# Optimization experiments

Measured on AMD Instinct MI355X. Metric: run time of the kernel, lower is better.

## Reference

```python
import jax, jax.numpy as jnp
import numpy as np

N = 50000      # nodes
E = 800000     # edges
D = 128        # input_dim = nb_hidden = emb_dim
A = 4          # nb_edge_types (edge attr dim)
H = 2          # heads (MyGATConv default)
G = 128        # number of graphs (g.batch)
NEG = 0.2      # leaky_relu negative slope
L = 3          # nb_layers


def _glorot(key, shape):
    lim = np.sqrt(6.0 / (shape[-2] + shape[-1]))
    return jax.random.uniform(key, shape, minval=-lim, maxval=lim, dtype=jnp.float32)


def setup_inputs():
    key = jax.random.key(0)
    ks = jax.random.split(key, 20)
    inp = {
        "x": jax.random.normal(ks[0], (N, D), jnp.float32),
        "edge_index": jax.random.randint(ks[1], (2, E), 0, N, dtype=jnp.int32),
        "edge_attr": jax.random.normal(ks[2], (E, A), jnp.float32),
        "batch": jnp.sort(jax.random.randint(ks[3], (N,), 0, G, dtype=jnp.int32)),
    }
    for l in range(L):
        inp[f"linN{l}"] = _glorot(ks[4 + 4 * l], (D, H * D))
        inp[f"linE{l}"] = _glorot(ks[5 + 4 * l], (A, H * A))
        inp[f"att{l}"] = _glorot(ks[6 + 4 * l], (1, H, 2 * D + A))
        inp[f"bias{l}"] = jnp.zeros((H * D,), jnp.float32)
    inp["fw"] = _glorot(ks[16], (D, 1))
    inp["fb"] = jnp.zeros((1,), jnp.float32)
    return inp


def _gat_layer(x_in, e_in, src, dst, linN, linE, att, bias):
    n = x_in.shape[0]
    x = (x_in @ linN + bias).reshape(n, H, D)              # [N,H,D]
    e = (e_in @ linE).reshape(-1, H, A)                    # [E,H,A]
    # alpha = (cat([x_i, x_j, e], -1) * att).sum(-1); x_i = x[src], x_j = x[dst]
    ai = jnp.einsum('nhc,hc->nh', x, att[0, :, :D])        # per-node, gathered at src
    aj = jnp.einsum('nhc,hc->nh', x, att[0, :, D:2 * D])   # per-node, gathered at dst
    ae = jnp.einsum('ehc,hc->eh', e, att[0, :, 2 * D:])
    alpha = jax.nn.leaky_relu(ai[src] + aj[dst] + ae, NEG)  # [E,H]
    # segment softmax over targets (edge_index[1])
    amax = jax.ops.segment_max(alpha, dst, num_segments=n)
    ex = jnp.exp(alpha - amax[dst])
    denom = jax.ops.segment_sum(ex, dst, num_segments=n)
    alpha = ex / denom[dst]
    # PyG propagate: message = alpha * x[src], scatter-add at dst
    msg = alpha[:, :, None] * x[src]                       # [E,H,D]
    out = jax.ops.segment_sum(msg, dst, num_segments=n) + x
    # concat=False -> mean over heads, then ReLU
    return jax.nn.relu(out.mean(axis=1)), jax.nn.relu(e.mean(axis=1))


def reference(x, edge_index, edge_attr, batch,
              linN0, linE0, att0, bias0,
              linN1, linE1, att1, bias1,
              linN2, linE2, att2, bias2,
              fw, fb):
    src, dst = edge_index[0], edge_index[1]
    params = [(linN0, linE0, att0, bias0),
              (linN1, linE1, att1, bias1),
              (linN2, linE2, att2, bias2)]
    h, e = x, edge_attr
    for (lN, lE, at, b) in params:
        h, e = _gat_layer(h, e, src, dst, lN, lE, at, b)
    pooled = jax.ops.segment_sum(h, batch, num_segments=G)  # global_add_pool -> [G,D]
    y = (pooled @ fw + fb).squeeze(-1)                      # [G]
    return y
```

## Files before the change

### kernel.cpp

```cpp
#include <hip/hip_runtime.h>
#include <hip/hip_bf16.h>

#define DD 128
#define AA 4
#define HH 2

typedef short short8 __attribute__((ext_vector_type(8)));
typedef float f32x4 __attribute__((ext_vector_type(4)));

__device__ inline unsigned short f2bf(float f) {
    unsigned u = __float_as_uint(f);
    unsigned r = (u + 0x7fffu + ((u >> 16) & 1u)) >> 16;
    return (unsigned short)r;
}
__device__ inline float4 unpack_bf16x4(uint2 v) {
    float4 r;
    r.x = __uint_as_float(v.x << 16);
    r.y = __uint_as_float(v.x & 0xffff0000u);
    r.z = __uint_as_float(v.y << 16);
    r.w = __uint_as_float(v.y & 0xffff0000u);
    return r;
}
__device__ inline uint2 pack_bf16x4(float a, float b, float c, float d) {
    uint2 p;
    p.x = (unsigned)f2bf(a) | ((unsigned)f2bf(b) << 16);
    p.y = (unsigned)f2bf(c) | ((unsigned)f2bf(d) << 16);
    return p;
}


__global__ void rank_kernel(const int* __restrict__ dst, int* __restrict__ cnt,
                            int* __restrict__ rank, int E) {
    int e = blockIdx.x * blockDim.x + threadIdx.x;
    if (e < E) rank[e] = atomicAdd(&cnt[dst[e]], 1);
}

__global__ __launch_bounds__(256) void scan1(const int* __restrict__ cnt,
                                             int* __restrict__ bsum, int N,
                                             float* __restrict__ y,
                                             const float* __restrict__ fb) {
    __shared__ int wsh[4];
    int b = blockIdx.x, t = threadIdx.x;
    int lane = t & 63, w = t >> 6;
    if (b == 0 && t < 128) y[t] = fb[0];
    int base = b * 1024;
    int v = 0;
    #pragma unroll
    for (int i = 0; i < 4; ++i) {
        int idx = base + i * 256 + t;
        v += (idx < N) ? cnt[idx] : 0;
    }
    #pragma unroll
    for (int o = 32; o; o >>= 1) v += __shfl_xor(v, o);
    if (lane == 0) wsh[w] = v;
    __syncthreads();
    if (t == 0) bsum[b] = wsh[0] + wsh[1] + wsh[2] + wsh[3];
}

__global__ __launch_bounds__(256) void scan3(const int* __restrict__ cnt,
                                             const int* __restrict__ bsum,
                                             int* __restrict__ row_off,
                                             int N, int NB, int E) {
    __shared__ int wtot[4];
    __shared__ int carry;
    int b = blockIdx.x, t = threadIdx.x;
    int lane = t & 63, w = t >> 6;
    if (w == 0) {
        int v = (lane < NB) ? bsum[lane] : 0;
        int x = v;
        #pragma unroll
        for (int o = 1; o < 64; o <<= 1) {
            int u = __shfl_up(x, o);
            if (lane >= o) x += u;
        }
        int base = (b == 0) ? 0 : __shfl(x, b - 1);
        if (lane == 0) carry = base;
    }
    if (b == 0 && t == 0) row_off[N] = E;
    __syncthreads();
    int base = b * 1024;
    #pragma unroll
    for (int it = 0; it < 4; ++it) {
        int idx = base + it * 256 + t;
        int v = (idx < N) ? cnt[idx] : 0;
        int x = v;
        #pragma unroll
        for (int o = 1; o < 64; o <<= 1) {
            int u = __shfl_up(x, o);
            if (lane >= o) x += u;
        }
        if (lane == 63) wtot[w] = x;
        __syncthreads();
        int woff = 0;
        for (int i = 0; i < w; ++i) woff += wtot[i];
        int c = carry;
        __syncthreads();
        if (t == 255) carry = c + woff + x;
        int ex = c + woff + x - v;
        if (idx < N) row_off[idx] = ex;
        __syncthreads();
    }
}

__global__ void perm_kernel(const int* __restrict__ src, const int* __restrict__ dst,
                            const int* __restrict__ rank,
                            const int* __restrict__ row_off,
                            int2* __restrict__ perm2, int E) {
    int e = blockIdx.x * blockDim.x + threadIdx.x;
    if (e >= E) return;
    int2 v; v.x = e; v.y = src[e];
    perm2[row_off[dst[e]] + rank[e]] = v;
}


__device__ inline void edge_stage(const float4& ev, const float* __restrict__ linE,
                                  const float* __restrict__ att, float2& ae, float4& enext) {
    float eh[8];
    #pragma unroll
    for (int c = 0; c < 8; ++c)
        eh[c] = ev.x * linE[c] + ev.y * linE[8 + c] + ev.z * linE[16 + c] + ev.w * linE[24 + c];
    float a0 = 0.f, a1 = 0.f;
    #pragma unroll
    for (int a = 0; a < 4; ++a) {
        a0 += eh[a]     * att[2 * DD + a];
        a1 += eh[4 + a] * att[(2 * DD + AA) + 2 * DD + a];
    }
    ae.x = a0; ae.y = a1;
    enext.x = fmaxf(0.5f * (eh[0] + eh[4]), 0.f);
    enext.y = fmaxf(0.5f * (eh[1] + eh[5]), 0.f);
    enext.z = fmaxf(0.5f * (eh[2] + eh[6]), 0.f);
    enext.w = fmaxf(0.5f * (eh[3] + eh[7]), 0.f);
}

__global__ __launch_bounds__(256) void prep_fused(
        const float* __restrict__ ein, const int2* __restrict__ perm2,
        const float* __restrict__ linE0, const float* __restrict__ att0,
        const float* __restrict__ linE1, const float* __restrict__ att1,
        const float* __restrict__ linE2, const float* __restrict__ att2,
        float2* __restrict__ ae0, float2* __restrict__ ae1, float2* __restrict__ ae2,
        int E, int ebE,
        const float* __restrict__ X, uint2* __restrict__ As, int N, int ebA,
        const float* __restrict__ W0, const float* __restrict__ W1,
        const float* __restrict__ W2, unsigned short* __restrict__ Bs) {
    int b = blockIdx.x;
    if (b < ebE) {
        int p = b * 256 + threadIdx.x;
        if (p >= E) return;
        int e = perm2[p].x;
        float4 ev = ((const float4*)ein)[e];
        float2 ae; float4 en;
        edge_stage(ev, linE0, att0, ae, en); ae0[p] = ae;
        edge_stage(en, linE1, att1, ae, ev); ae1[p] = ae;
        edge_stage(ev, linE2, att2, ae, en); ae2[p] = ae;
    } else if (b < ebE + ebA) {
        int t = (b - ebE) * 256 + threadIdx.x;
        if (t >= N * 32) return;
        int r = t >> 5, kq4 = t & 31;
        float4 v = ((const float4*)X)[t];
        int g = r >> 4, m = r & 15;
        int ks = kq4 >> 3, q = (kq4 >> 1) & 3;
        int cell = ((g * 4 + ks) * 4 + q) * 16 + m;
        As[cell * 2 + (kq4 & 1)] = pack_bf16x4(v.x, v.y, v.z, v.w);
    } else {
        int t = (b - ebE - ebA) * 256 + threadIdx.x;
        if (t >= 3 * 128 * 64) return;
        int l = t / (128 * 64);
        int r = t - l * (128 * 64);
        const float* W = (l == 0) ? W0 : (l == 1) ? W1 : W2;
        unsigned short* B = Bs + (size_t)l * 128 * 256;
        int k = r >> 6, c4g = r & 63;
        float4 v = ((const float4*)W)[r];
        int ct = c4g >> 2, n0 = (c4g & 3) * 4;
        int ks = k >> 5, q = (k >> 3) & 3, j = k & 7;
        int cellbase = ((ct * 4 + ks) * 4 + q) * 16 + n0;
        B[(cellbase + 0) * 8 + j] = f2bf(v.x);
        B[(cellbase + 1) * 8 + j] = f2bf(v.y);
        B[(cellbase + 2) * 8 + j] = f2bf(v.z);
        B[(cellbase + 3) * 8 + j] = f2bf(v.w);
    }
}


__global__ __launch_bounds__(256) void gemm_mfma(const short8* __restrict__ As,
                                                 const short8* __restrict__ Bs,
                                                 const float* __restrict__ bias,
                                                 const float* __restrict__ att,
                                                 uint2* __restrict__ xhb,
                                                 float* __restrict__ aiaj, int Ngroups) {
    __shared__ __align__(16) unsigned short sh[4][16 * 132];
    int w = threadIdx.x >> 6;
    int flat = blockIdx.x * 4 + w;
    int wid = flat >> 1, half = flat & 1;
    int lane = threadIdx.x & 63;
    if (wid >= Ngroups) return;
    int q = lane >> 4, m = lane & 15;

    const short8* Ag = As + (size_t)wid * 256;
    f32x4 acc[8];
    #pragma unroll
    for (int c8 = 0; c8 < 8; ++c8) acc[c8] = (f32x4){0.f, 0.f, 0.f, 0.f};

    #pragma unroll
    for (int ks = 0; ks < 4; ++ks) {
        short8 a = Ag[ks * 64 + lane];
        #pragma unroll
        for (int c8 = 0; c8 < 8; ++c8) {
            short8 b = Bs[(half * 8 + c8) * 256 + ks * 64 + lane];
            acc[c8] = __builtin_amdgcn_mfma_f32_16x16x32_bf16(a, b, acc[c8], 0, 0, 0);
        }
    }

    const float* atth = att + half * (2 * DD + AA);
    float ai[4] = {}, aj[4] = {};
    #pragma unroll
    for (int c8 = 0; c8 < 8; ++c8) {
        int col = c8 * 16 + m;
        float aS = atth[col];
        float aD = atth[DD + col];
        float bv = bias[(half * 8 + c8) * 16 + m];
        #pragma unroll
        for (int reg = 0; reg < 4; ++reg) {
            float val = acc[c8][reg] + bv;
            sh[w][(q * 4 + reg) * 132 + col] = f2bf(val);
            ai[reg] += val * aS;
            aj[reg] += val * aD;
        }
    }
    #pragma unroll
    for (int o = 1; o < 16; o <<= 1) {
        #pragma unroll
        for (int reg = 0; reg < 4; ++reg) {
            ai[reg] += __shfl_xor(ai[reg], o);
            aj[reg] += __shfl_xor(aj[reg], o);
        }
    }
    if (m == 0) {
        #pragma unroll
        for (int reg = 0; reg < 4; ++reg) {
            int row = wid * 16 + q * 4 + reg;
            aiaj[row * 4 + half] = ai[reg];
            aiaj[row * 4 + 2 + half] = aj[reg];
        }
    }
    #pragma unroll
    for (int r2 = 0; r2 < 8; ++r2) {
        int row = r2 * 2 + (lane >> 5);
        uint2 v = *(const uint2*)&sh[w][row * 132 + (lane & 31) * 4];
        xhb[(size_t)(wid * 16 + row) * 64 + half * 32 + (lane & 31)] = v;
    }
}


__global__ __launch_bounds__(256) void aggregate(const uint2* __restrict__ xhb,
                                                 const float* __restrict__ aiaj,
                                                 const float2* __restrict__ ae,
                                                 const int* __restrict__ row_off,
                                                 const int2* __restrict__ perm2,
                                                 uint2* __restrict__ hshuf,
                                                 const float* __restrict__ fw,
                                                 float* __restrict__ pdots, int N) {
    int w = threadIdx.x >> 6;
    int d = blockIdx.x * 4 + w;
    int lane = threadIdx.x & 63;
    if (d >= N) return;
    int s0 = row_off[d], s1 = row_off[d + 1];
    int deg = s1 - s0;
    const float2* aiaj2 = (const float2*)aiaj;
    float2 ajv = aiaj2[d * 2 + 1];
    float4 xd = unpack_bf16x4(xhb[(size_t)d * 64 + lane]);

    __shared__ float lex[4][64][2];
    __shared__ int lsrc[4][64];
    float4 acc = {0.f, 0.f, 0.f, 0.f};
    float den0 = 0.f, den1 = 0.f;
    int head = lane >> 5;

    for (int c = 0; c < deg; c += 64) {
        int n = min(64, deg - c);
        if (lane < n) {
            int p = s0 + c + lane;
            int s = perm2[p].y;
            float2 aiv = aiaj2[s * 2];
            float2 aev = ae[p];
            float a0 = aiv.x + ajv.x + aev.x; a0 = a0 > 0.f ? a0 : 0.2f * a0;
            float a1 = aiv.y + ajv.y + aev.y; a1 = a1 > 0.f ? a1 : 0.2f * a1;
            float e0 = __expf(a0), e1 = __expf(a1);
            den0 += e0; den1 += e1;
            lex[w][lane][0] = e0; lex[w][lane][1] = e1;
            lsrc[w][lane] = s;
        }
        #pragma unroll 8
        for (int j = 0; j < n; ++j) {
            float wgt = lex[w][j][head];
            float4 xv = unpack_bf16x4(xhb[(size_t)lsrc[w][j] * 64 + lane]);
            acc.x += wgt * xv.x; acc.y += wgt * xv.y;
            acc.z += wgt * xv.z; acc.w += wgt * xv.w;
        }
    }

    #pragma unroll
    for (int o = 32; o; o >>= 1) {
        den0 += __shfl_xor(den0, o);
        den1 += __shfl_xor(den1, o);
    }
    float den = head ? den1 : den0;
    if (deg == 0) den = 1.0f;
    float inv = 1.0f / den;

    float4 v;
    v.x = acc.x * inv + xd.x;
    v.y = acc.y * inv + xd.y;
    v.z = acc.z * inv + xd.z;
    v.w = acc.w * inv + xd.w;
    float4 o2;
    o2.x = __shfl_xor(v.x, 32);
    o2.y = __shfl_xor(v.y, 32);
    o2.z = __shfl_xor(v.z, 32);
    o2.w = __shfl_xor(v.w, 32);
    if (lane < 32) {
        float4 r;
        r.x = fmaxf(0.5f * (v.x + o2.x), 0.f);
        r.y = fmaxf(0.5f * (v.y + o2.y), 0.f);
        r.z = fmaxf(0.5f * (v.z + o2.z), 0.f);
        r.w = fmaxf(0.5f * (v.w + o2.w), 0.f);
        if (hshuf) {
            int g = d >> 4, m = d & 15;
            int ks = lane >> 3, q = (lane >> 1) & 3;
            int cell = ((g * 4 + ks) * 4 + q) * 16 + m;
            hshuf[cell * 2 + (lane & 1)] = pack_bf16x4(r.x, r.y, r.z, r.w);
        }
        if (pdots) {
            float4 wv = ((const float4*)fw)[lane];
            float pd = r.x * wv.x + r.y * wv.y + r.z * wv.z + r.w * wv.w;
            #pragma unroll
            for (int o = 16; o; o >>= 1) pd += __shfl_xor(pd, o);
            if (lane == 0) pdots[d] = pd;
        }
    }
}


__global__ __launch_bounds__(256) void segpool_kernel(const float* __restrict__ p,
                                                      const int* __restrict__ batch,
                                                      float* __restrict__ y, int N, int G) {
    __shared__ float bins[128];
    int t = threadIdx.x;
    if (t < G) bins[t] = 0.f;
    __syncthreads();
    int per = (N + gridDim.x - 1) / gridDim.x;
    int lo = blockIdx.x * per;
    int hi = min(lo + per, N);
    float acc = 0.f;
    int key = -1;
    for (int i = lo + t; i < hi; i += 256) {
        int k = batch[i];
        float v = p[i];
        if (k != key) {
            if (key >= 0) atomicAdd(&bins[key], acc);
            key = k;
            acc = 0.f;
        }
        acc += v;
    }
    if (key >= 0) atomicAdd(&bins[key], acc);
    __syncthreads();
    if (t < G && bins[t] != 0.f) atomicAdd(&y[t], bins[t]);
}


extern "C" void kernel_launch(void* const* d_in, const int* in_sizes, int n_in,
                              void* d_out, int out_size, void* d_ws, size_t ws_size,
                              hipStream_t stream) {
    const float* x     = (const float*)d_in[0];
    const int*   ei    = (const int*)d_in[1];
    const float* eattr = (const float*)d_in[2];
    const int*   batch = (const int*)d_in[3];
    const float* fw    = (const float*)d_in[16];
    const float* fb    = (const float*)d_in[17];
    float* y = (float*)d_out;

    const int N = in_sizes[0] / DD;
    const int E = in_sizes[1] / 2;
    const int G = out_size;

    const int* src = ei;
    const int* dst = ei + E;

    char* ws = (char*)d_ws;
    size_t off = 0;
    auto carve = [&](size_t bytes) {
        char* p = ws + off;
        off += (bytes + 255) & ~(size_t)255;
        return p;
    };
    uint2*  xhb     = (uint2*)carve((size_t)N * 256 * 2);
    uint2*  S0      = (uint2*)carve((size_t)N * 128 * 2);
    uint2*  S1      = (uint2*)carve((size_t)N * 128 * 2);
    unsigned short* Bs = (unsigned short*)carve((size_t)3 * 128 * 256 * 2);
    float2* ae0     = (float2*)carve((size_t)E * 2 * 4);
    float2* ae1     = (float2*)carve((size_t)E * 2 * 4);
    float2* ae2     = (float2*)carve((size_t)E * 2 * 4);
    float*  aiaj    = (float*)carve((size_t)N * 4 * 4);
    int*    row_off = (int*)carve((size_t)(N + 1) * 4);
    int*    cnt     = (int*)carve((size_t)N * 4);
    int*    rank    = (int*)carve((size_t)E * 4);
    int2*   perm2   = (int2*)carve((size_t)E * 8);
    float*  pdots   = (float*)carve((size_t)N * 4);
    int*    bsum    = (int*)carve((size_t)256 * 4);

    const int NB = (N + 1023) / 1024;
    const int Ngroups = N / 16;
    const int eb = (E + 255) / 256;

    hipMemsetAsync(cnt, 0, (size_t)N * 4, stream);
    rank_kernel<<<eb, 256, 0, stream>>>(dst, cnt, rank, E);
    scan1<<<NB, 256, 0, stream>>>(cnt, bsum, N, y, fb);
    scan3<<<NB, 256, 0, stream>>>(cnt, bsum, row_off, N, NB, E);
    perm_kernel<<<eb, 256, 0, stream>>>(src, dst, rank, row_off, perm2, E);

    const int ebA = (N * 32 + 255) / 256;
    const int ebW = (3 * 128 * 64 + 255) / 256;
    prep_fused<<<eb + ebA + ebW, 256, 0, stream>>>(
        eattr, perm2,
        (const float*)d_in[5], (const float*)d_in[6],
        (const float*)d_in[9], (const float*)d_in[10],
        (const float*)d_in[13], (const float*)d_in[14],
        ae0, ae1, ae2, E, eb,
        x, S0, N, ebA,
        (const float*)d_in[4], (const float*)d_in[8], (const float*)d_in[12], Bs);

    int gemm_blocks = (Ngroups * 2 + 3) / 4;
    int agg_blocks = (N + 3) / 4;
    float2* aes[3] = {ae0, ae1, ae2};
    uint2* Ain[3]  = {S0, S1, S0};
    uint2* Aout[3] = {S1, S0, nullptr};

    for (int l = 0; l < 3; ++l) {
        const float* att  = (const float*)d_in[6 + 4 * l];
        const float* bias = (const float*)d_in[7 + 4 * l];
        const short8* Bl  = (const short8*)(Bs + (size_t)l * 128 * 256);

        gemm_mfma<<<gemm_blocks, 256, 0, stream>>>((const short8*)Ain[l], Bl,
                                                   bias, att, xhb, aiaj, Ngroups);
        aggregate<<<agg_blocks, 256, 0, stream>>>(xhb, aiaj, aes[l], row_off, perm2,
                                                  Aout[l], fw, (l == 2) ? pdots : nullptr, N);
    }

    segpool_kernel<<<128, 256, 0, stream>>>(pdots, batch, y, N, G);
}
```

Measured before the change: 433.6 us.

## Split aggregation into denom pass and feature-sliced gather for cache locality

The GEMM output is now written as eight feature slices, each holding 16 columns per head, so one slice covers every node in a contiguous compact array. Aggregation becomes two kernels. The first computes the per-edge exp weights and per-node denominators, reading a new packed source-index array. The second launches 8× as many blocks, one per slice, and gathers neighbours with 8 edges in parallel per wave. The goal is to keep each slice's gather working set resident in L2 and to raise memory-level parallelism, at the cost of an extra launch, re-reading edge weights and indices per slice, and atomics for the final dot product.

```diff
diff --git a/kernel.cpp b/kernel.cpp
--- a/kernel.cpp
+++ b/kernel.cpp
@@ -137,6 +137,7 @@
         const float* __restrict__ linE0, const float* __restrict__ att0,
         const float* __restrict__ linE1, const float* __restrict__ att1,
         const float* __restrict__ linE2, const float* __restrict__ att2,
+        int* __restrict__ asrc,
         float2* __restrict__ ae0, float2* __restrict__ ae1, float2* __restrict__ ae2,
         int E, int ebE,
         const float* __restrict__ X, uint2* __restrict__ As, int N, int ebA,
@@ -146,8 +147,9 @@
     if (b < ebE) {
         int p = b * 256 + threadIdx.x;
         if (p >= E) return;
-        int e = perm2[p].x;
-        float4 ev = ((const float4*)ein)[e];
+        int2 pe = perm2[p];
+        asrc[p] = pe.y;
+        float4 ev = ((const float4*)ein)[pe.x];
         float2 ae; float4 en;
         edge_stage(ev, linE0, att0, ae, en); ae0[p] = ae;
         edge_stage(en, linE1, att1, ae, ev); ae1[p] = ae;
@@ -185,8 +187,8 @@
                                                  const short8* __restrict__ Bs,
                                                  const float* __restrict__ bias,
                                                  const float* __restrict__ att,
-                                                 uint2* __restrict__ xhb,
-                                                 float* __restrict__ aiaj, int Ngroups) {
+                                                 uint2* __restrict__ xslice,
+                                                 float* __restrict__ aiaj, int Ngroups, int N) {
     __shared__ __align__(16) unsigned short sh[4][16 * 132];
     int w = threadIdx.x >> 6;
     int flat = blockIdx.x * 4 + w;
@@ -242,23 +244,22 @@
             aiaj[row * 4 + 2 + half] = aj[reg];
         }
     }
-    #pragma unroll
-    for (int r2 = 0; r2 < 8; ++r2) {
-        int row = r2 * 2 + (lane >> 5);
-        uint2 v = *(const uint2*)&sh[w][row * 132 + (lane & 31) * 4];
-        xhb[(size_t)(wid * 16 + row) * 64 + half * 32 + (lane & 31)] = v;
-    }
-}
-
-
-__global__ __launch_bounds__(256) void aggregate(const uint2* __restrict__ xhb,
-                                                 const float* __restrict__ aiaj,
-                                                 const float2* __restrict__ ae,
-                                                 const int* __restrict__ row_off,
-                                                 const int2* __restrict__ perm2,
-                                                 uint2* __restrict__ hshuf,
-                                                 const float* __restrict__ fw,
-                                                 float* __restrict__ pdots, int N) {
+    int nl = lane >> 2, off = lane & 3;
+    #pragma unroll
+    for (int ct = 0; ct < 8; ++ct) {
+        uint2 v = *(const uint2*)&sh[w][nl * 132 + ct * 16 + off * 4];
+        xslice[((size_t)ct * N + wid * 16 + nl) * 8 + half * 4 + off] = v;
+    }
+}
+
+
+__global__ __launch_bounds__(256) void denom_kernel(const float* __restrict__ aiaj,
+                                                    const float2* __restrict__ ae,
+                                                    const int* __restrict__ row_off,
+                                                    const int* __restrict__ asrc,
+                                                    float2* __restrict__ alpha,
+                                                    float2* __restrict__ denom,
+                                                    float* __restrict__ pdots, int N) {
     int w = threadIdx.x >> 6;
     int d = blockIdx.x * 4 + w;
     int lane = threadIdx.x & 63;
@@ -267,74 +268,108 @@
     int deg = s1 - s0;
     const float2* aiaj2 = (const float2*)aiaj;
     float2 ajv = aiaj2[d * 2 + 1];
-    float4 xd = unpack_bf16x4(xhb[(size_t)d * 64 + lane]);
-
-    __shared__ float lex[4][64][2];
-    __shared__ int lsrc[4][64];
-    float4 acc = {0.f, 0.f, 0.f, 0.f};
     float den0 = 0.f, den1 = 0.f;
-    int head = lane >> 5;
-
     for (int c = 0; c < deg; c += 64) {
-        int n = min(64, deg - c);
-        if (lane < n) {
+        if (c + lane < deg) {
             int p = s0 + c + lane;
-            int s = perm2[p].y;
+            int s = asrc[p];
             float2 aiv = aiaj2[s * 2];
             float2 aev = ae[p];
             float a0 = aiv.x + ajv.x + aev.x; a0 = a0 > 0.f ? a0 : 0.2f * a0;
             float a1 = aiv.y + ajv.y + aev.y; a1 = a1 > 0.f ? a1 : 0.2f * a1;
             float e0 = __expf(a0), e1 = __expf(a1);
             den0 += e0; den1 += e1;
-            lex[w][lane][0] = e0; lex[w][lane][1] = e1;
-            lsrc[w][lane] = s;
-        }
-        #pragma unroll 8
-        for (int j = 0; j < n; ++j) {
-            float wgt = lex[w][j][head];
-            float4 xv = unpack_bf16x4(xhb[(size_t)lsrc[w][j] * 64 + lane]);
-            acc.x += wgt * xv.x; acc.y += wgt * xv.y;
-            acc.z += wgt * xv.z; acc.w += wgt * xv.w;
-        }
-    }
-
+            float2 al; al.x = e0; al.y = e1;
+            alpha[p] = al;
+        }
+    }
     #pragma unroll
     for (int o = 32; o; o >>= 1) {
         den0 += __shfl_xor(den0, o);
         den1 += __shfl_xor(den1, o);
     }
-    float den = head ? den1 : den0;
-    if (deg == 0) den = 1.0f;
-    float inv = 1.0f / den;
-
+    if (lane == 0) {
+        float2 dn;
+        dn.x = (deg == 0) ? 1.f : den0;
+        dn.y = (deg == 0) ? 1.f : den1;
+        denom[d] = dn;
+        if (pdots) pdots[d] = 0.f;
+    }
+}
+
+
+__global__ __launch_bounds__(256) void agg_slice(const uint2* __restrict__ xslice,
+                                                 const float2* __restrict__ alpha,
+                                                 const int* __restrict__ asrc,
+                                                 const int* __restrict__ row_off,
+                                                 const float2* __restrict__ denom,
+                                                 uint2* __restrict__ hshuf,
+                                                 const float* __restrict__ fw,
+                                                 float* __restrict__ pdots, int N) {
+    int b = blockIdx.x;
+    int s = b & 7;
+    int w = threadIdx.x >> 6;
+    int d = (b >> 3) * 4 + w;
+    int lane = threadIdx.x & 63;
+    if (d >= N) return;
+    int eg = lane >> 3, f = lane & 7;
+    int s0 = row_off[d], s1 = row_off[d + 1];
+    int deg = s1 - s0;
+    const uint2* Xs = xslice + (size_t)s * N * 8;
+    float4 xd = unpack_bf16x4(Xs[(size_t)d * 8 + f]);
+
+    float4 acc = {0.f, 0.f, 0.f, 0.f};
+    for (int c = 0; c < deg; c += 8) {
+        float2 w2 = {0.f, 0.f};
+        int sn = 0;
+        if (c + eg < deg) {
+            int p = s0 + c + eg;
+            w2 = alpha[p];
+            sn = asrc[p];
+        }
+        float wgt = (f < 4) ? w2.x : w2.y;
+        float4 xv = unpack_bf16x4(Xs[(size_t)sn * 8 + f]);
+        acc.x += wgt * xv.x; acc.y += wgt * xv.y;
+        acc.z += wgt * xv.z; acc.w += wgt * xv.w;
+    }
+    #pragma unroll
+    for (int o = 8; o < 64; o <<= 1) {
+        acc.x += __shfl_xor(acc.x, o);
+        acc.y += __shfl_xor(acc.y, o);
+        acc.z += __shfl_xor(acc.z, o);
+        acc.w += __shfl_xor(acc.w, o);
+    }
+    float2 dn = denom[d];
+    float inv = 1.0f / ((f < 4) ? dn.x : dn.y);
     float4 v;
     v.x = acc.x * inv + xd.x;
     v.y = acc.y * inv + xd.y;
     v.z = acc.z * inv + xd.z;
     v.w = acc.w * inv + xd.w;
     float4 o2;
-    o2.x = __shfl_xor(v.x, 32);
-    o2.y = __shfl_xor(v.y, 32);
-    o2.z = __shfl_xor(v.z, 32);
-    o2.w = __shfl_xor(v.w, 32);
-    if (lane < 32) {
+    o2.x = __shfl_xor(v.x, 4);
+    o2.y = __shfl_xor(v.y, 4);
+    o2.z = __shfl_xor(v.z, 4);
+    o2.w = __shfl_xor(v.w, 4);
+    if (lane < 4) {
         float4 r;
         r.x = fmaxf(0.5f * (v.x + o2.x), 0.f);
         r.y = fmaxf(0.5f * (v.y + o2.y), 0.f);
         r.z = fmaxf(0.5f * (v.z + o2.z), 0.f);
         r.w = fmaxf(0.5f * (v.w + o2.w), 0.f);
+        int L = s * 4 + lane;
         if (hshuf) {
             int g = d >> 4, m = d & 15;
-            int ks = lane >> 3, q = (lane >> 1) & 3;
+            int ks = L >> 3, q = (L >> 1) & 3, bb = L & 1;
             int cell = ((g * 4 + ks) * 4 + q) * 16 + m;
-            hshuf[cell * 2 + (lane & 1)] = pack_bf16x4(r.x, r.y, r.z, r.w);
+            hshuf[cell * 2 + bb] = pack_bf16x4(r.x, r.y, r.z, r.w);
         }
         if (pdots) {
-            float4 wv = ((const float4*)fw)[lane];
+            float4 wv = ((const float4*)fw)[L];
             float pd = r.x * wv.x + r.y * wv.y + r.z * wv.z + r.w * wv.w;
-            #pragma unroll
-            for (int o = 16; o; o >>= 1) pd += __shfl_xor(pd, o);
-            if (lane == 0) pdots[d] = pd;
+            pd += __shfl_xor(pd, 1);
+            pd += __shfl_xor(pd, 2);
+            if (lane == 0) atomicAdd(&pdots[d], pd);
         }
     }
 }
@@ -393,18 +428,21 @@
         off += (bytes + 255) & ~(size_t)255;
         return p;
     };
-    uint2*  xhb     = (uint2*)carve((size_t)N * 256 * 2);
+    uint2*  xslice  = (uint2*)carve((size_t)N * 64 * 8);
     uint2*  S0      = (uint2*)carve((size_t)N * 128 * 2);
     uint2*  S1      = (uint2*)carve((size_t)N * 128 * 2);
     unsigned short* Bs = (unsigned short*)carve((size_t)3 * 128 * 256 * 2);
     float2* ae0     = (float2*)carve((size_t)E * 2 * 4);
     float2* ae1     = (float2*)carve((size_t)E * 2 * 4);
     float2* ae2     = (float2*)carve((size_t)E * 2 * 4);
+    float2* alpha   = (float2*)carve((size_t)E * 8);
     float*  aiaj    = (float*)carve((size_t)N * 4 * 4);
+    float2* denomb  = (float2*)carve((size_t)N * 8);
     int*    row_off = (int*)carve((size_t)(N + 1) * 4);
     int*    cnt     = (int*)carve((size_t)N * 4);
     int*    rank    = (int*)carve((size_t)E * 4);
     int2*   perm2   = (int2*)carve((size_t)E * 8);
+    int*    asrc    = (int*)carve((size_t)E * 4);
     float*  pdots   = (float*)carve((size_t)N * 4);
     int*    bsum    = (int*)carve((size_t)256 * 4);
 
@@ -425,12 +463,13 @@
         (const float*)d_in[5], (const float*)d_in[6],
         (const float*)d_in[9], (const float*)d_in[10],
         (const float*)d_in[13], (const float*)d_in[14],
-        ae0, ae1, ae2, E, eb,
+        asrc, ae0, ae1, ae2, E, eb,
         x, S0, N, ebA,
         (const float*)d_in[4], (const float*)d_in[8], (const float*)d_in[12], Bs);
 
     int gemm_blocks = (Ngroups * 2 + 3) / 4;
-    int agg_blocks = (N + 3) / 4;
+    int nd_blocks = (N + 3) / 4;
+    int slice_blocks = nd_blocks * 8;
     float2* aes[3] = {ae0, ae1, ae2};
     uint2* Ain[3]  = {S0, S1, S0};
     uint2* Aout[3] = {S1, S0, nullptr};
@@ -439,11 +478,14 @@
         const float* att  = (const float*)d_in[6 + 4 * l];
         const float* bias = (const float*)d_in[7 + 4 * l];
         const short8* Bl  = (const short8*)(Bs + (size_t)l * 128 * 256);
+        float* pd = (l == 2) ? pdots : nullptr;
 
         gemm_mfma<<<gemm_blocks, 256, 0, stream>>>((const short8*)Ain[l], Bl,
-                                                   bias, att, xhb, aiaj, Ngroups);
-        aggregate<<<agg_blocks, 256, 0, stream>>>(xhb, aiaj, aes[l], row_off, perm2,
-                                                  Aout[l], fw, (l == 2) ? pdots : nullptr, N);
+                                                   bias, att, xslice, aiaj, Ngroups, N);
+        denom_kernel<<<nd_blocks, 256, 0, stream>>>(aiaj, aes[l], row_off, asrc,
+                                                    alpha, denomb, pd, N);
+        agg_slice<<<slice_blocks, 256, 0, stream>>>(xslice, alpha, asrc, row_off,
+                                                    denomb, Aout[l], fw, pd, N);
     }
 
     segpool_kernel<<<128, 256, 0, stream>>>(pdots, batch, y, N, G);
```

Result: slower. 769.6 us (+77.5%).

## Gather two neighbors per wave with 16-byte loads and compact source index array

Applied to the files above, without the earlier changes.

The aggregation loop now has each half-wave handle a different neighbor, with each lane loading 16 bytes (8 bf16) instead of 8. That halves the number of serial gather iterations per edge chunk, and the half-wave partial sums are combined with a cross-half shuffle. The chunk is padded with a zero-weight dummy edge so the count can be rounded up to even. Separately, source indices are written to a compact int array during prep, so aggregate no longer reads the 8-byte perm2 pairs. The cost is more registers for the 8 accumulators and extra shuffles in the epilogue.

```diff
diff --git a/kernel.cpp b/kernel.cpp
--- a/kernel.cpp
+++ b/kernel.cpp
@@ -137,6 +137,7 @@
         const float* __restrict__ linE0, const float* __restrict__ att0,
         const float* __restrict__ linE1, const float* __restrict__ att1,
         const float* __restrict__ linE2, const float* __restrict__ att2,
+        int* __restrict__ asrc,
         float2* __restrict__ ae0, float2* __restrict__ ae1, float2* __restrict__ ae2,
         int E, int ebE,
         const float* __restrict__ X, uint2* __restrict__ As, int N, int ebA,
@@ -146,8 +147,9 @@
     if (b < ebE) {
         int p = b * 256 + threadIdx.x;
         if (p >= E) return;
-        int e = perm2[p].x;
-        float4 ev = ((const float4*)ein)[e];
+        int2 pe = perm2[p];
+        asrc[p] = pe.y;
+        float4 ev = ((const float4*)ein)[pe.x];
         float2 ae; float4 en;
         edge_stage(ev, linE0, att0, ae, en); ae0[p] = ae;
         edge_stage(en, linE1, att1, ae, ev); ae1[p] = ae;
@@ -255,7 +257,7 @@
                                                  const float* __restrict__ aiaj,
                                                  const float2* __restrict__ ae,
                                                  const int* __restrict__ row_off,
-                                                 const int2* __restrict__ perm2,
+                                                 const int* __restrict__ asrc,
                                                  uint2* __restrict__ hshuf,
                                                  const float* __restrict__ fw,
                                                  float* __restrict__ pdots, int N) {
@@ -267,19 +269,24 @@
     int deg = s1 - s0;
     const float2* aiaj2 = (const float2*)aiaj;
     float2 ajv = aiaj2[d * 2 + 1];
-    float4 xd = unpack_bf16x4(xhb[(size_t)d * 64 + lane]);
+    const uint4* X4 = (const uint4*)xhb;
+
+    int half = lane >> 5;
+    int li = lane & 31;
+    int headp = li >> 4;
+
+    uint4 xdp = X4[(size_t)d * 32 + li];
 
     __shared__ float lex[4][64][2];
     __shared__ int lsrc[4][64];
-    float4 acc = {0.f, 0.f, 0.f, 0.f};
+    float a[8] = {};
     float den0 = 0.f, den1 = 0.f;
-    int head = lane >> 5;
 
     for (int c = 0; c < deg; c += 64) {
         int n = min(64, deg - c);
         if (lane < n) {
             int p = s0 + c + lane;
-            int s = perm2[p].y;
+            int s = asrc[p];
             float2 aiv = aiaj2[s * 2];
             float2 aev = ae[p];
             float a0 = aiv.x + ajv.x + aev.x; a0 = a0 > 0.f ? a0 : 0.2f * a0;
@@ -288,52 +295,71 @@
             den0 += e0; den1 += e1;
             lex[w][lane][0] = e0; lex[w][lane][1] = e1;
             lsrc[w][lane] = s;
-        }
-        #pragma unroll 8
-        for (int j = 0; j < n; ++j) {
-            float wgt = lex[w][j][head];
-            float4 xv = unpack_bf16x4(xhb[(size_t)lsrc[w][j] * 64 + lane]);
-            acc.x += wgt * xv.x; acc.y += wgt * xv.y;
-            acc.z += wgt * xv.z; acc.w += wgt * xv.w;
-        }
-    }
-
+        } else if (lane == n) {
+            lex[w][lane][0] = 0.f; lex[w][lane][1] = 0.f;
+            lsrc[w][lane] = 0;
+        }
+        int n2 = (n + 1) & ~1;
+        for (int j = 0; j < n2; j += 2) {
+            float wgt = lex[w][j + half][headp];
+            int sn = lsrc[w][j + half];
+            uint4 xv = X4[(size_t)sn * 32 + li];
+            a[0] += wgt * __uint_as_float(xv.x << 16);
+            a[1] += wgt * __uint_as_float(xv.x & 0xffff0000u);
+            a[2] += wgt * __uint_as_float(xv.y << 16);
+            a[3] += wgt * __uint_as_float(xv.y & 0xffff0000u);
+            a[4] += wgt * __uint_as_float(xv.z << 16);
+            a[5] += wgt * __uint_as_float(xv.z & 0xffff0000u);
+            a[6] += wgt * __uint_as_float(xv.w << 16);
+            a[7] += wgt * __uint_as_float(xv.w & 0xffff0000u);
+        }
+    }
+
+    #pragma unroll
+    for (int k = 0; k < 8; ++k) a[k] += __shfl_xor(a[k], 32);
     #pragma unroll
     for (int o = 32; o; o >>= 1) {
         den0 += __shfl_xor(den0, o);
         den1 += __shfl_xor(den1, o);
     }
-    float den = head ? den1 : den0;
+    float den = headp ? den1 : den0;
     if (deg == 0) den = 1.0f;
     float inv = 1.0f / den;
 
-    float4 v;
-    v.x = acc.x * inv + xd.x;
-    v.y = acc.y * inv + xd.y;
-    v.z = acc.z * inv + xd.z;
-    v.w = acc.w * inv + xd.w;
-    float4 o2;
-    o2.x = __shfl_xor(v.x, 32);
-    o2.y = __shfl_xor(v.y, 32);
-    o2.z = __shfl_xor(v.z, 32);
-    o2.w = __shfl_xor(v.w, 32);
-    if (lane < 32) {
-        float4 r;
-        r.x = fmaxf(0.5f * (v.x + o2.x), 0.f);
-        r.y = fmaxf(0.5f * (v.y + o2.y), 0.f);
-        r.z = fmaxf(0.5f * (v.z + o2.z), 0.f);
-        r.w = fmaxf(0.5f * (v.w + o2.w), 0.f);
+    float v[8];
+    v[0] = a[0] * inv + __uint_as_float(xdp.x << 16);
+    v[1] = a[1] * inv + __uint_as_float(xdp.x & 0xffff0000u);
+    v[2] = a[2] * inv + __uint_as_float(xdp.y << 16);
+    v[3] = a[3] * inv + __uint_as_float(xdp.y & 0xffff0000u);
+    v[4] = a[4] * inv + __uint_as_float(xdp.z << 16);
+    v[5] = a[5] * inv + __uint_as_float(xdp.z & 0xffff0000u);
+    v[6] = a[6] * inv + __uint_as_float(xdp.w << 16);
+    v[7] = a[7] * inv + __uint_as_float(xdp.w & 0xffff0000u);
+
+    float r[8];
+    #pragma unroll
+    for (int k = 0; k < 8; ++k) {
+        float o2 = __shfl_xor(v[k], 16);
+        r[k] = fmaxf(0.5f * (v[k] + o2), 0.f);
+    }
+    if (lane < 16) {
         if (hshuf) {
             int g = d >> 4, m = d & 15;
-            int ks = lane >> 3, q = (lane >> 1) & 3;
-            int cell = ((g * 4 + ks) * 4 + q) * 16 + m;
-            hshuf[cell * 2 + (lane & 1)] = pack_bf16x4(r.x, r.y, r.z, r.w);
+            int L0 = lane * 2, L1 = L0 + 1;
+            int ks0 = L0 >> 3, q0 = (L0 >> 1) & 3;
+            int cell0 = ((g * 4 + ks0) * 4 + q0) * 16 + m;
+            hshuf[cell0 * 2 + 0] = pack_bf16x4(r[0], r[1], r[2], r[3]);
+            int ks1 = L1 >> 3, q1 = (L1 >> 1) & 3;
+            int cell1 = ((g * 4 + ks1) * 4 + q1) * 16 + m;
+            hshuf[cell1 * 2 + 1] = pack_bf16x4(r[4], r[5], r[6], r[7]);
         }
         if (pdots) {
-            float4 wv = ((const float4*)fw)[lane];
-            float pd = r.x * wv.x + r.y * wv.y + r.z * wv.z + r.w * wv.w;
+            const float4* fw4 = (const float4*)fw;
+            float4 w0 = fw4[lane * 2], w1 = fw4[lane * 2 + 1];
+            float pd = r[0] * w0.x + r[1] * w0.y + r[2] * w0.z + r[3] * w0.w
+                     + r[4] * w1.x + r[5] * w1.y + r[6] * w1.z + r[7] * w1.w;
             #pragma unroll
-            for (int o = 16; o; o >>= 1) pd += __shfl_xor(pd, o);
+            for (int o = 8; o; o >>= 1) pd += __shfl_xor(pd, o);
             if (lane == 0) pdots[d] = pd;
         }
     }
@@ -405,6 +431,7 @@
     int*    cnt     = (int*)carve((size_t)N * 4);
     int*    rank    = (int*)carve((size_t)E * 4);
     int2*   perm2   = (int2*)carve((size_t)E * 8);
+    int*    asrc    = (int*)carve((size_t)E * 4);
     float*  pdots   = (float*)carve((size_t)N * 4);
     int*    bsum    = (int*)carve((size_t)256 * 4);
 
@@ -425,7 +452,7 @@
         (const float*)d_in[5], (const float*)d_in[6],
         (const float*)d_in[9], (const float*)d_in[10],
         (const float*)d_in[13], (const float*)d_in[14],
-        ae0, ae1, ae2, E, eb,
+        asrc, ae0, ae1, ae2, E, eb,
         x, S0, N, ebA,
         (const float*)d_in[4], (const float*)d_in[8], (const float*)d_in[12], Bs);
 
@@ -442,7 +469,7 @@
 
         gemm_mfma<<<gemm_blocks, 256, 0, stream>>>((const short8*)Ain[l], Bl,
                                                    bias, att, xhb, aiaj, Ngroups);
-        aggregate<<<agg_blocks, 256, 0, stream>>>(xhb, aiaj, aes[l], row_off, perm2,
+        aggregate<<<agg_blocks, 256, 0, stream>>>(xhb, aiaj, aes[l], row_off, asrc,
                                                   Aout[l], fw, (l == 2) ? pdots : nullptr, N);
     }
 
```

New measurement: 431.3 us. Within noise of the previous version (-0.5%).
